# Kernel optimization log

Measured on AMD Instinct MI355X. Metric: run time of the kernel, lower is better.

Reference implementation:

```python
import jax, jax.numpy as jnp
import numpy as np

B, C, T, L, H = 4, 512, 8, 512, 8


def _normalize(a, eps=1e-12):
    # F.normalize: x / max(||x||_2, eps) along last dim
    n = jnp.linalg.norm(a, axis=-1, keepdims=True)
    return a / jnp.maximum(n, eps)


def setup_inputs() -> dict:
    key = jax.random.key(0)
    ks = jax.random.split(key, 8)
    w = lambda k, shp: (jax.random.normal(k, shp, dtype=jnp.float32) * 0.02)
    return {
        "e": jax.random.normal(ks[0], (B, C, T, L), dtype=jnp.float32),
        "x": jax.random.normal(ks[1], (B, C, T, L), dtype=jnp.float32),
        "Wq": w(ks[2], (C, C)), "bq": jnp.zeros((C,), jnp.float32),
        "Wkv": w(ks[3], (2 * C, C)), "bkv": jnp.zeros((2 * C,), jnp.float32),
        "Wm": w(ks[4], (C, C)), "bm": jnp.zeros((C,), jnp.float32),
        "Wg1": w(ks[5], (C, C)), "bg1": jnp.zeros((C,), jnp.float32),
        "Wg2": w(ks[6], (H, C)), "bg2": jnp.zeros((H,), jnp.float32),
    }


def reference(e, x, Wq, bq, Wkv, bkv, Wm, bm, Wg1, bg1, Wg2, bg2):
    shortcut = x
    xp = jnp.transpose(x, (0, 2, 3, 1))  # (b,t,l,c)
    ep = jnp.transpose(e, (0, 2, 3, 1))  # (b,t,l,c)
    b, t, l, c = xp.shape
    hd = c // H

    # per-(b,t) head gating from pooled e (gate_weights1 == gate_weights in source)
    pooled = ep.mean(axis=2)  # (b,t,c)
    glog = jnp.tanh(pooled @ Wg1.T + bg1) @ Wg2.T + bg2  # (b,t,H)
    gw = jax.nn.softmax(glog, axis=-1)[..., None, None]  # (b,t,H,1,1)

    q = (ep @ Wq.T + bq).reshape(b, t, l, H, hd).transpose(0, 1, 3, 2, 4)  # (b,t,H,l,hd)
    q = _normalize(q)
    kv = (xp @ Wkv.T + bkv).reshape(b, t, l, 2 * H, hd).transpose(0, 1, 3, 2, 4)
    k, v = kv[:, :, :H], kv[:, :, H:]
    k = _normalize(k)
    v = _normalize(v) * gw  # pre-softmax value gating

    scale = jnp.float32(1.0 / np.sqrt(hd))
    att = jax.nn.softmax(jnp.einsum('bthid,bthjd->bthij', q, k) * scale, axis=-1)
    o = jnp.einsum('bthij,bthjd->bthid', att, v) * gw  # post-attention gating

    o = o.transpose(0, 1, 3, 2, 4).reshape(b, t, l, c)
    o = o @ Wm.T + bm
    return jnp.transpose(o, (0, 3, 1, 2)) + shortcut
```

## Files before the change

### kernel.cpp

```cpp
#include <hip/hip_runtime.h>
#include <math.h>

#define B_ 4
#define C_ 512
#define T_ 8
#define L_ 512
#define H_ 8
#define HD_ 64

typedef unsigned short ushort_t;
using short8 = __attribute__((ext_vector_type(8))) short;
using f4 = __attribute__((ext_vector_type(4))) float;

#define GLOAD_LDS(gp, lp)                                                      \
  __builtin_amdgcn_global_load_lds(                                            \
      (const __attribute__((address_space(1))) unsigned int*)(gp),             \
      (__attribute__((address_space(3))) unsigned int*)(lp), 16, 0, 0)

__device__ __forceinline__ unsigned pack_bf16(float a, float b) {
  union { float f; unsigned u; } ua, ub;
  ua.f = a; ub.f = b;
  unsigned ra = (ua.u + 0x7FFFu + ((ua.u >> 16) & 1u)) >> 16;
  unsigned rb = (ub.u + 0x7FFFu + ((ub.u >> 16) & 1u)) >> 16;
  return (rb << 16) | (ra & 0xFFFFu);
}
__device__ __forceinline__ ushort_t bf16_1(float a) {
  union { float f; unsigned u; } ua; ua.f = a;
  return (ushort_t)((ua.u + 0x7FFFu + ((ua.u >> 16) & 1u)) >> 16);
}


__global__ __launch_bounds__(256) void gate1_kernel(const float* __restrict__ pooled,
                                                    const float* __restrict__ Wg1,
                                                    const float* __restrict__ bg1,
                                                    float* __restrict__ h1) {
  int w = threadIdx.x >> 6, lane = threadIdx.x & 63;
  int row = blockIdx.x * 4 + w;
  int bt = blockIdx.y;
  const float* wr = Wg1 + (size_t)row * C_;
  const float* pr = pooled + bt * C_;
  float s = 0.f;
#pragma unroll
  for (int i = 0; i < 8; ++i) s += wr[lane + i * 64] * pr[lane + i * 64];
#pragma unroll
  for (int off = 32; off > 0; off >>= 1) s += __shfl_down(s, off, 64);
  if (lane == 0) h1[bt * C_ + row] = tanhf(s + bg1[row]);
}

__global__ __launch_bounds__(256) void gate2_kernel(const float* __restrict__ h1,
                                                    const float* __restrict__ Wg2,
                                                    const float* __restrict__ bg2,
                                                    float* __restrict__ gwp) {
  __shared__ float part[256];
  __shared__ float gl[H_];
  int bt = blockIdx.x, tid = threadIdx.x;
  int h = tid >> 5, s = tid & 31;
  const float* w2 = Wg2 + (size_t)h * C_;
  const float* hb = h1 + bt * C_;
  float p = 0.f;
  for (int c = s; c < C_; c += 32) p += w2[c] * hb[c];
  part[tid] = p;
  __syncthreads();
  if (tid < H_) {
    float a = bg2[tid];
    for (int i = 0; i < 32; ++i) a += part[tid * 32 + i];
    gl[tid] = a;
  }
  __syncthreads();
  if (tid == 0) {
    float m = -1e30f;
    for (int i = 0; i < H_; ++i) m = fmaxf(m, gl[i]);
    float sum = 0.f;
    float ex[H_];
    for (int i = 0; i < H_; ++i) { ex[i] = expf(gl[i] - m); sum += ex[i]; }
    for (int i = 0; i < H_; ++i) gwp[bt * H_ + i] = ex[i] / sum;
  }
}

__global__ __launch_bounds__(256) void cvt_kernel(const float* __restrict__ s,
                                                  ushort_t* __restrict__ d) {
  int i = (blockIdx.x * 256 + threadIdx.x) * 8;
  float4 a = *(const float4*)(s + i);
  float4 b = *(const float4*)(s + i + 4);
  uint4 o;
  o.x = pack_bf16(a.x, a.y); o.y = pack_bf16(a.z, a.w);
  o.z = pack_bf16(b.x, b.y); o.w = pack_bf16(b.z, b.w);
  *(uint4*)(d + i) = o;
}

__global__ __launch_bounds__(256) void tconv_kernel(const float* __restrict__ src,
                                                    ushort_t* __restrict__ dst,
                                                    float* __restrict__ pooled) {
  __shared__ float tb[64][65];
  int tid = threadIdx.x;
  int b = blockIdx.z >> 3, t = blockIdx.z & 7;
  int c0 = blockIdx.y * 64, l0 = blockIdx.x * 64;
  const float* sp = src + (((size_t)(b * C_ + c0) * T_) + t) * L_ + l0;
  int j = tid & 63, i0 = tid >> 6;
#pragma unroll
  for (int p = 0; p < 16; ++p) {
    int i = p * 4 + i0;
    tb[i][j] = sp[(size_t)i * (T_ * L_) + j];
  }
  __syncthreads();
  if (pooled) {
    int c = tid >> 2, part = tid & 3;
    float s = 0.f;
#pragma unroll
    for (int k = 0; k < 16; ++k) s += tb[c][part * 16 + k];
    s += __shfl_down(s, 1);
    s += __shfl_down(s, 2);
    if (part == 0) atomicAdd(&pooled[blockIdx.z * C_ + c0 + c], s * (1.0f / L_));
  }
  int ii = (tid & 31) * 2, jj0 = tid >> 5;
  ushort_t* dp = dst + ((size_t)blockIdx.z * L_ + l0) * C_ + c0;
#pragma unroll
  for (int p = 0; p < 8; ++p) {
    int jj = p * 8 + jj0;
    *(unsigned*)(dp + (size_t)jj * C_ + ii) = pack_bf16(tb[ii][jj], tb[ii + 1][jj]);
  }
}

__global__ __launch_bounds__(256, 2) void gemm_mfma(
    const ushort_t* __restrict__ A, const ushort_t* __restrict__ BT,
    const float* __restrict__ bias, int mode,
    float* __restrict__ Out, const float* __restrict__ resid,
    ushort_t* __restrict__ Kdst, ushort_t* __restrict__ Vdst,
    const float* __restrict__ gwp, float qscale) {
  __shared__ alignas(16) ushort_t As[128 * 32];
  __shared__ alignas(16) ushort_t Bs[128 * 32];
  int tid = threadIdx.x;
  int w = tid >> 6, lane = tid & 63, l15 = lane & 15, q = lane >> 4;
  int n0 = blockIdx.x * 128, m0 = blockIdx.y * 128, bt = blockIdx.z;
  int wm = (w >> 1) * 64, wn = (w & 1) * 64;
  const ushort_t* Bbt = BT + (size_t)bt * C_ * C_;

  int c0 = w * 64 + lane, c1 = 256 + w * 64 + lane;
  const ushort_t* ag0 = A + (size_t)(m0 + (c0 >> 2)) * 512 + (c0 & 3) * 8;
  const ushort_t* ag1 = A + (size_t)(m0 + (c1 >> 2)) * 512 + (c1 & 3) * 8;
  const ushort_t* bg0 = Bbt + (size_t)(n0 + (c0 >> 2)) * 512 + (c0 & 3) * 8;
  const ushort_t* bg1 = Bbt + (size_t)(n0 + (c1 >> 2)) * 512 + (c1 & 3) * 8;
  ushort_t* la0 = As + (size_t)(w * 64) * 8;
  ushort_t* la1 = As + (size_t)(256 + w * 64) * 8;
  ushort_t* lb0 = Bs + (size_t)(w * 64) * 8;
  ushort_t* lb1 = Bs + (size_t)(256 + w * 64) * 8;

  f4 acc[4][4];
#pragma unroll
  for (int i = 0; i < 4; ++i)
#pragma unroll
    for (int j = 0; j < 4; ++j) acc[i][j] = (f4){0.f, 0.f, 0.f, 0.f};

  for (int k0 = 0; k0 < 512; k0 += 32) {
    __syncthreads();
    GLOAD_LDS(ag0 + k0, la0);
    GLOAD_LDS(ag1 + k0, la1);
    GLOAD_LDS(bg0 + k0, lb0);
    GLOAD_LDS(bg1 + k0, lb1);
    __syncthreads();
    short8 af[4], bf[4];
#pragma unroll
    for (int mt = 0; mt < 4; ++mt)
      af[mt] = *(const short8*)&As[(size_t)(wm + mt * 16 + l15) * 32 + q * 8];
#pragma unroll
    for (int nt = 0; nt < 4; ++nt)
      bf[nt] = *(const short8*)&Bs[(size_t)(wn + nt * 16 + l15) * 32 + q * 8];
#pragma unroll
    for (int mt = 0; mt < 4; ++mt)
#pragma unroll
      for (int nt = 0; nt < 4; ++nt)
        acc[mt][nt] =
            __builtin_amdgcn_mfma_f32_16x16x32_bf16(af[mt], bf[nt], acc[mt][nt], 0, 0, 0);
  }

#pragma unroll
  for (int mt = 0; mt < 4; ++mt)
#pragma unroll
    for (int r = 0; r < 4; ++r) {
      float bb = bias[m0 + wm + mt * 16 + q * 4 + r];
#pragma unroll
      for (int nt = 0; nt < 4; ++nt) acc[mt][nt][r] += bb;
    }

  if (mode == 0) {
    int b = bt >> 3, t = bt & 7;
    float* Ob = Out + (size_t)b * (C_ * T_ * L_) + (size_t)t * L_;
    const float* Rb = resid + (size_t)b * (C_ * T_ * L_) + (size_t)t * L_;
#pragma unroll
    for (int mt = 0; mt < 4; ++mt)
#pragma unroll
      for (int r = 0; r < 4; ++r) {
        size_t ro = (size_t)(m0 + wm + mt * 16 + q * 4 + r) * (T_ * L_);
#pragma unroll
        for (int nt = 0; nt < 4; ++nt) {
          int n = n0 + wn + nt * 16 + l15;
          Ob[ro + n] = acc[mt][nt][r] + Rb[ro + n];
        }
      }
    return;
  }

  float scale[4];
#pragma unroll
  for (int nt = 0; nt < 4; ++nt) {
    float s = 0.f;
#pragma unroll
    for (int mt = 0; mt < 4; ++mt)
#pragma unroll
      for (int r = 0; r < 4; ++r) s += acc[mt][nt][r] * acc[mt][nt][r];
    s += __shfl_xor(s, 16);
    s += __shfl_xor(s, 32);
    scale[nt] = s;
  }
  int hh = ((m0 + wm) >> 6) & 7;
  bool isv = (mode == 2) && (m0 + wm >= 512);
  float mult = isv ? gwp[bt * H_ + hh] : qscale;
#pragma unroll
  for (int nt = 0; nt < 4; ++nt)
    scale[nt] = mult / fmaxf(sqrtf(scale[nt]), 1e-12f);

  if (!isv) {
    ushort_t* Kb = Kdst + (size_t)(bt * H_ + hh) * 512 * 64;
#pragma unroll
    for (int nt = 0; nt < 4; ++nt) {
      int l = n0 + wn + nt * 16 + l15;
      ushort_t* rowp = Kb + (size_t)l * 64;
#pragma unroll
      for (int mt = 0; mt < 4; ++mt) {
        uint2 pk;
        pk.x = pack_bf16(acc[mt][nt][0] * scale[nt], acc[mt][nt][1] * scale[nt]);
        pk.y = pack_bf16(acc[mt][nt][2] * scale[nt], acc[mt][nt][3] * scale[nt]);
        *(uint2*)&rowp[mt * 16 + q * 4] = pk;
      }
    }
  } else {
    ushort_t* Vb = Vdst + (size_t)(bt * H_ + hh) * 64 * 512;
#pragma unroll
    for (int mt = 0; mt < 4; ++mt)
#pragma unroll
      for (int r = 0; r < 4; ++r) {
        int d = mt * 16 + q * 4 + r;
        ushort_t* rp = Vb + (size_t)d * 512 + n0 + wn;
#pragma unroll
        for (int nt = 0; nt < 4; ++nt)
          rp[nt * 16 + l15] = bf16_1(acc[mt][nt][r] * scale[nt]);
      }
  }
}

__global__ __launch_bounds__(512, 2) void attn_kernel(
    const ushort_t* __restrict__ Qbf, const ushort_t* __restrict__ Kbf,
    const ushort_t* __restrict__ Vbf, const float* __restrict__ gwp,
    ushort_t* __restrict__ obfT) {
  int tid = threadIdx.x;
  int w = tid >> 6, lane = tid & 63, l15 = lane & 15, q = lane >> 4;
  int h = blockIdx.x, bt = blockIdx.y;

  const ushort_t* Qg = Qbf + (size_t)(bt * H_ + h) * 512 * 64;
  const ushort_t* Kg = Kbf + (size_t)(bt * H_ + h) * 512 * 64;
  const ushort_t* Vg = Vbf + (size_t)(bt * H_ + h) * 64 * 512;

  short8 qf[4][2];
#pragma unroll
  for (int f = 0; f < 4; ++f) {
    const ushort_t* qrow = Qg + (size_t)(w * 64 + f * 16 + l15) * 64;
    qf[f][0] = *(const short8*)&qrow[q * 8];
    qf[f][1] = *(const short8*)&qrow[32 + q * 8];
  }

  f4 acc[4][4];
#pragma unroll
  for (int f = 0; f < 4; ++f)
#pragma unroll
    for (int dt = 0; dt < 4; ++dt) acc[f][dt] = (f4){0.f, 0.f, 0.f, 0.f};
  float lsum[4] = {0.f, 0.f, 0.f, 0.f};
  bool hi_half = (lane >= 32);
  int qh2 = (q & 1) * 2;

  for (int j0 = 0; j0 < 512; j0 += 64) {
    short8 kf[4][2], vf[2][4];
#pragma unroll
    for (int jt = 0; jt < 4; ++jt) {
      const ushort_t* krow = Kg + (size_t)(j0 + jt * 16 + l15) * 64;
      kf[jt][0] = *(const short8*)&krow[q * 8];
      kf[jt][1] = *(const short8*)&krow[32 + q * 8];
    }
#pragma unroll
    for (int ks2 = 0; ks2 < 2; ++ks2)
#pragma unroll
      for (int dt = 0; dt < 4; ++dt)
        vf[ks2][dt] = *(const short8*)(Vg + (size_t)(dt * 16 + l15) * 512 + j0 +
                                       ks2 * 32 + q * 8);

#pragma unroll
    for (int f = 0; f < 4; ++f) {
      f4 sc[4];
#pragma unroll
      for (int jt = 0; jt < 4; ++jt) {
        f4 c = {0.f, 0.f, 0.f, 0.f};
        c = __builtin_amdgcn_mfma_f32_16x16x32_bf16(kf[jt][0], qf[f][0], c, 0, 0, 0);
        c = __builtin_amdgcn_mfma_f32_16x16x32_bf16(kf[jt][1], qf[f][1], c, 0, 0, 0);
        sc[jt] = c;
      }
      float ls = 0.f;
#pragma unroll
      for (int jt = 0; jt < 4; ++jt)
#pragma unroll
        for (int r = 0; r < 4; ++r) {
          float p = __expf(sc[jt][r]);
          sc[jt][r] = p;
          ls += p;
        }
      lsum[f] += ls;

      unsigned pk01[4], pk23[4];
#pragma unroll
      for (int jt = 0; jt < 4; ++jt) {
        pk01[jt] = pack_bf16(sc[jt][0], sc[jt][1]);
        pk23[jt] = pack_bf16(sc[jt][2], sc[jt][3]);
      }
#pragma unroll
      for (int ks2 = 0; ks2 < 2; ++ks2) {
        union { unsigned u[4]; short8 s; } bu;
#pragma unroll
        for (int r = 0; r < 4; ++r) {
          int src = (qh2 + (r >> 1)) * 16 + l15;
          unsigned pl = (r & 1) ? pk23[ks2 * 2] : pk01[ks2 * 2];
          unsigned ph = (r & 1) ? pk23[ks2 * 2 + 1] : pk01[ks2 * 2 + 1];
          unsigned lo = __shfl(pl, src);
          unsigned hi = __shfl(ph, src);
          bu.u[r] = hi_half ? hi : lo;
        }
#pragma unroll
        for (int dt = 0; dt < 4; ++dt)
          acc[f][dt] = __builtin_amdgcn_mfma_f32_16x16x32_bf16(vf[ks2][dt], bu.s,
                                                               acc[f][dt], 0, 0, 0);
      }
    }
  }

  float g = gwp[bt * H_ + h];
#pragma unroll
  for (int f = 0; f < 4; ++f) {
    float ls = lsum[f];
    ls += __shfl_xor(ls, 16);
    ls += __shfl_xor(ls, 32);
    float inv = g / ls;
    int iglob = w * 64 + f * 16 + l15;
    ushort_t* ob = obfT + ((size_t)(bt * 512 + iglob)) * 512 + h * 64;
#pragma unroll
    for (int dt = 0; dt < 4; ++dt) {
      uint2 pk;
      pk.x = pack_bf16(acc[f][dt][0] * inv, acc[f][dt][1] * inv);
      pk.y = pack_bf16(acc[f][dt][2] * inv, acc[f][dt][3] * inv);
      *(uint2*)&ob[dt * 16 + q * 4] = pk;
    }
  }
}

extern "C" void kernel_launch(void* const* d_in, const int* in_sizes, int n_in,
                              void* d_out, int out_size, void* d_ws, size_t ws_size,
                              hipStream_t stream) {
  const float* e   = (const float*)d_in[0];
  const float* x   = (const float*)d_in[1];
  const float* Wq  = (const float*)d_in[2];
  const float* bq  = (const float*)d_in[3];
  const float* Wkv = (const float*)d_in[4];
  const float* bkv = (const float*)d_in[5];
  const float* Wm  = (const float*)d_in[6];
  const float* bm  = (const float*)d_in[7];
  const float* Wg1 = (const float*)d_in[8];
  const float* bg1 = (const float*)d_in[9];
  const float* Wg2 = (const float*)d_in[10];
  const float* bg2 = (const float*)d_in[11];
  float* out = (float*)d_out;

  float* ws = (float*)d_ws;
  float* pooled = ws;
  float* gwp    = ws + 16384;
  float* h1buf  = ws + 16640;
  float* fb     = ws + 33024;
  ushort_t* ebfT = (ushort_t*)(fb);
  ushort_t* xbfT = (ushort_t*)(fb + 1 * 4194304);
  ushort_t* Qbf  = (ushort_t*)(fb + 2 * 4194304);
  ushort_t* Kbf  = (ushort_t*)(fb + 3 * 4194304);
  ushort_t* Vbf  = (ushort_t*)(fb + 4 * 4194304);
  ushort_t* obfT = (ushort_t*)(fb + 5 * 4194304);
  ushort_t* Wqb  = (ushort_t*)(fb + 6 * 4194304);
  ushort_t* Wkvb = Wqb + 262144;
  ushort_t* Wmb  = Wkvb + 524288;

  hipMemsetAsync(pooled, 0, 16384 * sizeof(float), stream);
  cvt_kernel<<<dim3(128), dim3(256), 0, stream>>>(Wq, Wqb);
  cvt_kernel<<<dim3(256), dim3(256), 0, stream>>>(Wkv, Wkvb);
  cvt_kernel<<<dim3(128), dim3(256), 0, stream>>>(Wm, Wmb);
  tconv_kernel<<<dim3(8, 8, 32), dim3(256), 0, stream>>>(e, ebfT, pooled);
  tconv_kernel<<<dim3(8, 8, 32), dim3(256), 0, stream>>>(x, xbfT, nullptr);
  gate1_kernel<<<dim3(128, 32), dim3(256), 0, stream>>>(pooled, Wg1, bg1, h1buf);
  gate2_kernel<<<dim3(32), dim3(256), 0, stream>>>(h1buf, Wg2, bg2, gwp);
  gemm_mfma<<<dim3(4, 4, 32), dim3(256), 0, stream>>>(
      Wqb, ebfT, bq, 1, nullptr, nullptr, Qbf, nullptr, gwp, 0.125f);
  gemm_mfma<<<dim3(4, 8, 32), dim3(256), 0, stream>>>(
      Wkvb, xbfT, bkv, 2, nullptr, nullptr, Kbf, Vbf, gwp, 1.0f);
  attn_kernel<<<dim3(H_, 32), dim3(512), 0, stream>>>(Qbf, Kbf, Vbf, gwp, obfT);
  gemm_mfma<<<dim3(4, 4, 32), dim3(256), 0, stream>>>(
      Wmb, obfT, bm, 0, out, x, nullptr, nullptr, gwp, 1.0f);
}
```

Measured before the change: 260.3 us.

## Merge Q and KV projection GEMMs into one launch; split attention query rows

```diff
diff --git a/kernel.cpp b/kernel.cpp
--- a/kernel.cpp
+++ b/kernel.cpp
@@ -122,17 +122,32 @@
 }
 
 __global__ __launch_bounds__(256, 2) void gemm_mfma(
-    const ushort_t* __restrict__ A, const ushort_t* __restrict__ BT,
-    const float* __restrict__ bias, int mode,
-    float* __restrict__ Out, const float* __restrict__ resid,
-    ushort_t* __restrict__ Kdst, ushort_t* __restrict__ Vdst,
-    const float* __restrict__ gwp, float qscale) {
+    const ushort_t* __restrict__ Aq, const ushort_t* __restrict__ BTq,
+    const float* __restrict__ biasq, const ushort_t* __restrict__ Akv,
+    const ushort_t* __restrict__ BTkv, const float* __restrict__ biaskv,
+    int mode, float* __restrict__ Out, const float* __restrict__ resid,
+    ushort_t* __restrict__ Qdst, ushort_t* __restrict__ Kdst,
+    ushort_t* __restrict__ Vdst, const float* __restrict__ gwp) {
   __shared__ alignas(16) ushort_t As[128 * 32];
   __shared__ alignas(16) ushort_t Bs[128 * 32];
   int tid = threadIdx.x;
   int w = tid >> 6, lane = tid & 63, l15 = lane & 15, q = lane >> 4;
-  int n0 = blockIdx.x * 128, m0 = blockIdx.y * 128, bt = blockIdx.z;
+  int n0 = blockIdx.x * 128, bt = blockIdx.z;
   int wm = (w >> 1) * 64, wn = (w & 1) * 64;
+
+  const ushort_t* A;
+  const ushort_t* BT;
+  const float* bias;
+  int m0, lmode;
+  if (mode == 3) {
+    if (blockIdx.y < 4) {
+      A = Aq; BT = BTq; bias = biasq; lmode = 1; m0 = blockIdx.y * 128;
+    } else {
+      A = Akv; BT = BTkv; bias = biaskv; lmode = 2; m0 = (blockIdx.y - 4) * 128;
+    }
+  } else {
+    A = Aq; BT = BTq; bias = biasq; lmode = 0; m0 = blockIdx.y * 128;
+  }
   const ushort_t* Bbt = BT + (size_t)bt * C_ * C_;
 
   int c0 = w * 64 + lane, c1 = 256 + w * 64 + lane;
@@ -182,7 +197,7 @@
       for (int nt = 0; nt < 4; ++nt) acc[mt][nt][r] += bb;
     }
 
-  if (mode == 0) {
+  if (lmode == 0) {
     int b = bt >> 3, t = bt & 7;
     float* Ob = Out + (size_t)b * (C_ * T_ * L_) + (size_t)t * L_;
     const float* Rb = resid + (size_t)b * (C_ * T_ * L_) + (size_t)t * L_;
@@ -213,18 +228,18 @@
     scale[nt] = s;
   }
   int hh = ((m0 + wm) >> 6) & 7;
-  bool isv = (mode == 2) && (m0 + wm >= 512);
-  float mult = isv ? gwp[bt * H_ + hh] : qscale;
+  bool isv = (lmode == 2) && (m0 + wm >= 512);
+  float mult = isv ? gwp[bt * H_ + hh] : (lmode == 1 ? 0.125f : 1.0f);
 #pragma unroll
   for (int nt = 0; nt < 4; ++nt)
     scale[nt] = mult / fmaxf(sqrtf(scale[nt]), 1e-12f);
 
   if (!isv) {
-    ushort_t* Kb = Kdst + (size_t)(bt * H_ + hh) * 512 * 64;
+    ushort_t* Db = (lmode == 1 ? Qdst : Kdst) + (size_t)(bt * H_ + hh) * 512 * 64;
 #pragma unroll
     for (int nt = 0; nt < 4; ++nt) {
       int l = n0 + wn + nt * 16 + l15;
-      ushort_t* rowp = Kb + (size_t)l * 64;
+      ushort_t* rowp = Db + (size_t)l * 64;
 #pragma unroll
       for (int mt = 0; mt < 4; ++mt) {
         uint2 pk;
@@ -248,32 +263,33 @@
   }
 }
 
-__global__ __launch_bounds__(512, 2) void attn_kernel(
+__global__ __launch_bounds__(512, 4) void attn_kernel(
     const ushort_t* __restrict__ Qbf, const ushort_t* __restrict__ Kbf,
     const ushort_t* __restrict__ Vbf, const float* __restrict__ gwp,
     ushort_t* __restrict__ obfT) {
   int tid = threadIdx.x;
   int w = tid >> 6, lane = tid & 63, l15 = lane & 15, q = lane >> 4;
-  int h = blockIdx.x, bt = blockIdx.y;
+  int qb = blockIdx.x, h = blockIdx.y, bt = blockIdx.z;
+  int iw = qb * 256 + w * 32;
 
   const ushort_t* Qg = Qbf + (size_t)(bt * H_ + h) * 512 * 64;
   const ushort_t* Kg = Kbf + (size_t)(bt * H_ + h) * 512 * 64;
   const ushort_t* Vg = Vbf + (size_t)(bt * H_ + h) * 64 * 512;
 
-  short8 qf[4][2];
-#pragma unroll
-  for (int f = 0; f < 4; ++f) {
-    const ushort_t* qrow = Qg + (size_t)(w * 64 + f * 16 + l15) * 64;
+  short8 qf[2][2];
+#pragma unroll
+  for (int f = 0; f < 2; ++f) {
+    const ushort_t* qrow = Qg + (size_t)(iw + f * 16 + l15) * 64;
     qf[f][0] = *(const short8*)&qrow[q * 8];
     qf[f][1] = *(const short8*)&qrow[32 + q * 8];
   }
 
-  f4 acc[4][4];
-#pragma unroll
-  for (int f = 0; f < 4; ++f)
+  f4 acc[2][4];
+#pragma unroll
+  for (int f = 0; f < 2; ++f)
 #pragma unroll
     for (int dt = 0; dt < 4; ++dt) acc[f][dt] = (f4){0.f, 0.f, 0.f, 0.f};
-  float lsum[4] = {0.f, 0.f, 0.f, 0.f};
+  float lsum[2] = {0.f, 0.f};
   bool hi_half = (lane >= 32);
   int qh2 = (q & 1) * 2;
 
@@ -293,7 +309,7 @@
                                        ks2 * 32 + q * 8);
 
 #pragma unroll
-    for (int f = 0; f < 4; ++f) {
+    for (int f = 0; f < 2; ++f) {
       f4 sc[4];
 #pragma unroll
       for (int jt = 0; jt < 4; ++jt) {
@@ -341,12 +357,12 @@
 
   float g = gwp[bt * H_ + h];
 #pragma unroll
-  for (int f = 0; f < 4; ++f) {
+  for (int f = 0; f < 2; ++f) {
     float ls = lsum[f];
     ls += __shfl_xor(ls, 16);
     ls += __shfl_xor(ls, 32);
     float inv = g / ls;
-    int iglob = w * 64 + f * 16 + l15;
+    int iglob = iw + f * 16 + l15;
     ushort_t* ob = obfT + ((size_t)(bt * 512 + iglob)) * 512 + h * 64;
 #pragma unroll
     for (int dt = 0; dt < 4; ++dt) {
@@ -398,11 +414,10 @@
   tconv_kernel<<<dim3(8, 8, 32), dim3(256), 0, stream>>>(x, xbfT, nullptr);
   gate1_kernel<<<dim3(128, 32), dim3(256), 0, stream>>>(pooled, Wg1, bg1, h1buf);
   gate2_kernel<<<dim3(32), dim3(256), 0, stream>>>(h1buf, Wg2, bg2, gwp);
+  gemm_mfma<<<dim3(4, 12, 32), dim3(256), 0, stream>>>(
+      Wqb, ebfT, bq, Wkvb, xbfT, bkv, 3, nullptr, nullptr, Qbf, Kbf, Vbf, gwp);
+  attn_kernel<<<dim3(2, H_, 32), dim3(512), 0, stream>>>(Qbf, Kbf, Vbf, gwp, obfT);
   gemm_mfma<<<dim3(4, 4, 32), dim3(256), 0, stream>>>(
-      Wqb, ebfT, bq, 1, nullptr, nullptr, Qbf, nullptr, gwp, 0.125f);
-  gemm_mfma<<<dim3(4, 8, 32), dim3(256), 0, stream>>>(
-      Wkvb, xbfT, bkv, 2, nullptr, nullptr, Kbf, Vbf, gwp, 1.0f);
-  attn_kernel<<<dim3(H_, 32), dim3(512), 0, stream>>>(Qbf, Kbf, Vbf, gwp, obfT);
-  gemm_mfma<<<dim3(4, 4, 32), dim3(256), 0, stream>>>(
-      Wmb, obfT, bm, 0, out, x, nullptr, nullptr, gwp, 1.0f);
-}
+      Wmb, obfT, bm, nullptr, nullptr, nullptr, 0, out, x, nullptr, nullptr,
+      nullptr, gwp);
+}
```

After: 280.5 us. 7.8% more time.
